# Kernel optimization log

Hardware: AMD Instinct MI355X
Metric: run time of the kernel (lower is better)

## Reference

```python
import jax, jax.numpy as jnp
import numpy as np

B, S, D = 2, 1024, 768
NH = 12
DH = D // NH
HID = 1536
G, EPG = 4, 2
E = G * EPG
TEMP = 1.0
LN_EPS = 1e-5


def setup_inputs() -> dict:
    key = jax.random.key(0)
    ks = jax.random.split(key, 8)
    s = 0.02
    return {
        "x": jax.random.normal(ks[0], (B, S, D), jnp.float32),
        "ln1_w": jnp.ones((D,), jnp.float32),
        "ln1_b": jnp.zeros((D,), jnp.float32),
        "in_proj_w": jax.random.normal(ks[1], (3 * D, D), jnp.float32) * s,
        "in_proj_b": jnp.zeros((3 * D,), jnp.float32),
        "out_proj_w": jax.random.normal(ks[2], (D, D), jnp.float32) * s,
        "out_proj_b": jnp.zeros((D,), jnp.float32),
        "ln2_w": jnp.ones((D,), jnp.float32),
        "ln2_b": jnp.zeros((D,), jnp.float32),
        "Wg": jax.random.normal(ks[3], (D, G), jnp.float32) * s,
        "bg": jnp.zeros((G,), jnp.float32),
        "We": jax.random.normal(ks[4], (G, D, EPG), jnp.float32) * s,
        "be": jnp.zeros((G, EPG), jnp.float32),
        "W1": jax.random.normal(ks[5], (E, D, HID), jnp.float32) * s,
        "b1": jnp.zeros((E, HID), jnp.float32),
        "W2": jax.random.normal(ks[6], (E, HID, D), jnp.float32) * s,
        "b2": jnp.zeros((E, D), jnp.float32),
    }


def _ln(x, w, b):
    m = x.mean(-1, keepdims=True)
    v = x.var(-1, keepdims=True)
    return (x - m) / jnp.sqrt(v + LN_EPS) * w + b


def _mha(h, wqkv, bqkv, wo, bo):
    qkv = h @ wqkv.T + bqkv                       # [B,S,3D]
    q, k, v = jnp.split(qkv, 3, axis=-1)
    q = q.reshape(B, S, NH, DH)
    k = k.reshape(B, S, NH, DH)
    v = v.reshape(B, S, NH, DH)
    scale = 1.0 / np.sqrt(DH).astype(np.float32)
    att = jnp.einsum("bqhd,bkhd->bhqk", q, k) * scale
    p = jax.nn.softmax(att, axis=-1)
    o = jnp.einsum("bhqk,bkhd->bqhd", p, v).reshape(B, S, D)
    return o @ wo.T + bo


def _moe(h, Wg, bg, We, be, W1, b1, W2, b2):
    hf = h.reshape(-1, D)                         # [N,D] tokens
    # level-1: group router (temperature softmax, top-1)
    gp = jax.nn.softmax((hf @ Wg + bg) / TEMP, axis=-1)          # [N,G]
    g = jnp.argmax(gp, axis=-1)                                   # [N]
    pg = jnp.take_along_axis(gp, g[:, None], axis=1)[:, 0]        # [N]
    # level-2: within-group expert router
    el = jnp.einsum("nd,gde->nge", hf, We) + be                   # [N,G,EPG]
    ep = jax.nn.softmax(el / TEMP, axis=-1)
    ep_g = jnp.take_along_axis(ep, g[:, None, None], axis=1)[:, 0, :]  # [N,EPG]
    e = jnp.argmax(ep_g, axis=-1)                                 # [N]
    pe = jnp.take_along_axis(ep_g, e[:, None], axis=1)[:, 0]      # [N]
    flat = g * EPG + e                                            # flat expert id [N]
    combine = jax.nn.one_hot(flat, E, dtype=hf.dtype) * (pg * pe)[:, None]  # [N,E]
    # dense expert compute (reference form of dispatch/grouped-GEMM/combine)
    hid = jax.nn.gelu(jnp.einsum("nd,edh->enh", hf, W1) + b1[:, None, :])   # [E,N,HID]
    y = jnp.einsum("enh,ehd->end", hid, W2) + b2[:, None, :]                # [E,N,D]
    out = jnp.einsum("ne,end->nd", combine, y)                              # [N,D]
    return out.reshape(h.shape)


def reference(x, ln1_w, ln1_b, in_proj_w, in_proj_b, out_proj_w, out_proj_b,
              ln2_w, ln2_b, Wg, bg, We, be, W1, b1, W2, b2):
    a = _mha(_ln(x, ln1_w, ln1_b), in_proj_w, in_proj_b, out_proj_w, out_proj_b)
    x = x + a  # dropout p=0.0 -> identity
    m = _moe(_ln(x, ln2_w, ln2_b), Wg, bg, We, be, W1, b1, W2, b2)
    return x + m
```

## Files before the change

### kernel.cpp

```cpp
#include <hip/hip_runtime.h>
#include <stdint.h>

#define B_ 2
#define S_ 1024
#define D_ 768
#define NH_ 12
#define DH_ 64
#define HID_ 1536
#define G_ 4
#define EPG_ 2
#define E_ 8
#define NTOK (B_*S_)
#define NGRP (B_*NH_*16)

typedef unsigned short u16;
typedef unsigned int u32;
typedef __bf16 bf16x8 __attribute__((ext_vector_type(8)));
typedef float f32x4 __attribute__((ext_vector_type(4)));
typedef u16 u16x4 __attribute__((ext_vector_type(4)));
typedef u32 u32x4 __attribute__((ext_vector_type(4)));

struct BfPair { u16 hi, lo; };

__device__ __forceinline__ u16 f2bf(float f){
// ... 46 lines not shown
    const float* src; u16* dst; int R, C, cx, cy, e;
    if (bid < 11520){
      int r = bid - 2304; e = r / 1152; r %= 1152;
      R = D_; C = HID_; cx = r % 48; cy = r / 48;
      src = W1; dst = W1t;
    } else {
      int r = bid - 11520; e = r / 1152; r %= 1152;
      R = HID_; C = D_; cx = r % 24; cy = r / 24;
      src = W2; dst = W2t;
    }
    const float* s = src + (size_t)e * R * C;
    u16* d = dst + (size_t)e * R * C;
    int c0 = cx * 32, r0 = cy * 32;
    int tx = t & 31, ty = t >> 5;
    #pragma unroll
    for (int i = 0; i < 32; i += 8)
      tile[ty + i][tx] = s[(size_t)(r0 + ty + i) * C + c0 + tx];
    __syncthreads();
    #pragma unroll
    for (int i = 0; i < 32; i += 8)
      d[(size_t)(c0 + ty + i) * R + r0 + tx] = f2bf(tile[tx][ty + i]);
  }
}

__global__ void k_transpose_v(const u16* __restrict__ qh, const u16* __restrict__ ql,
                              u16* __restrict__ vth, u16* __restrict__ vtl){
  __shared__ u16 th[32][34], tl[32][34];
  int bh = blockIdx.z, b = bh / NH_, h = bh % NH_;
  int d0 = blockIdx.x * 32, s0 = blockIdx.y * 32;
  #pragma unroll
  for (int i = 0; i < 32; i += 8){
    size_t src = (size_t)(b * S_ + s0 + threadIdx.y + i) * (3 * D_) + 2 * D_ + h * DH_ + d0 + threadIdx.x;
    th[threadIdx.y + i][threadIdx.x] = qh[src];
    tl[threadIdx.y + i][threadIdx.x] = ql[src];
  }
  __syncthreads();
  #pragma unroll
  for (int i = 0; i < 32; i += 8){
    size_t dst = ((size_t)bh * DH_ + d0 + threadIdx.y + i) * S_ + s0 + threadIdx.x;
    vth[dst] = th[threadIdx.x][threadIdx.y + i];
    vtl[dst] = tl[threadIdx.x][threadIdx.y + i];
  }
}

__global__ __launch_bounds__(256) void k_layernorm(
    const float* __restrict__ x, const float* __restrict__ w, const float* __restrict__ b,
    u16* __restrict__ oh, u16* __restrict__ ol, float* __restrict__ of){
  int row = blockIdx.x;
  const float* xr = x + (size_t)row * D_;
  int t = threadIdx.x;
  float v0 = xr[t], v1 = xr[t + 256], v2 = xr[t + 512];
  float s = v0 + v1 + v2;
  float sq = v0 * v0 + v1 * v1 + v2 * v2;
  #pragma unroll
  for (int m = 1; m < 64; m <<= 1){ s += __shfl_xor(s, m); sq += __shfl_xor(sq, m); }
  __shared__ float ls[4], lq[4];
  int wid = t >> 6;
  if ((t & 63) == 0){ ls[wid] = s; lq[wid] = sq; }
  __syncthreads();
  s = ls[0] + ls[1] + ls[2] + ls[3];
  sq = lq[0] + lq[1] + lq[2] + lq[3];
  float mean = s * (1.f / D_);
  float var = sq * (1.f / D_) - mean * mean;
  float rstd = rsqrtf(var + 1e-5f);
  #pragma unroll
  for (int i = 0; i < 3; i++){
    int dcol = t + i * 256;
    float v = (i == 0 ? v0 : (i == 1 ? v1 : v2));
    float y = (v - mean) * rstd * w[dcol] + b[dcol];
    BfPair p = split_bf(y);
    oh[(size_t)row * D_ + dcol] = p.hi;
    if (ol) ol[(size_t)row * D_ + dcol] = p.lo;
    if (of) of[(size_t)row * D_ + dcol] = y;
  }
}

template<int EPI>
__global__ __launch_bounds__(256) void k_gemm3(
    const u16* __restrict__ Ah, const u16* __restrict__ Al,
    const u16* __restrict__ Bh, const u16* __restrict__ Bl,
    const float* __restrict__ bias, const float* __restrict__ resid,
    u16* __restrict__ outh, u16* __restrict__ outl, float* __restrict__ outf,
    int M, int N, int K){
  __shared__ alignas(16) u16 Ash[2][64 * 32];
  __shared__ alignas(16) u16 Asl[2][64 * 32];
  __shared__ alignas(16) u16 Bsh[2][64 * 32];
  __shared__ alignas(16) u16 Bsl[2][64 * 32];
  int m0 = blockIdx.x * 64, n0 = blockIdx.y * 64;
  int tid = threadIdx.x, w = tid >> 6, l = tid & 63;
  int wr = w >> 1, wc = w & 1;
  f32x4 acc[2][2];
  #pragma unroll
  for (int i = 0; i < 2; i++)
    #pragma unroll
    for (int j = 0; j < 2; j++) acc[i][j] = f32x4{0.f, 0.f, 0.f, 0.f};
  int srow = w * 16 + (l >> 2);
  int scol = 8 * ((l & 3) ^ ((l >> 2) & 3));
  const u16* gAh = Ah + (size_t)(m0 + srow) * K + scol;
  const u16* gAl = Al + (size_t)(m0 + srow) * K + scol;
  const u16* gBh = Bh + (size_t)(n0 + srow) * K + scol;
  const u16* gBl = Bl + (size_t)(n0 + srow) * K + scol;
  int dOff = (w * 16) * 32;
  auto STAGE = [&](int buf, int k0){
    gload_lds16(gAh + k0, &Ash[buf][dOff]);
    gload_lds16(gAl + k0, &Asl[buf][dOff]);
    gload_lds16(gBh + k0, &Bsh[buf][dOff]);
    gload_lds16(gBl + k0, &Bsl[buf][dOff]);
  };
  STAGE(0, 0);
  __syncthreads();
  int nk = K / 32;
  int ca = (l >> 4) ^ (l & 3);
  int ai = (wr * 32 + (l & 15)) * 32 + 8 * ca;
  int bi = (wc * 32 + (l & 15)) * 32 + 8 * ca;
  for (int t = 0; t < nk; t++){
    int cur = t & 1;
    if (t + 1 < nk) STAGE(cur ^ 1, (t + 1) * 32);
    bf16x8 afh[2], afl[2], bfh[2], bfl[2];
    #pragma unroll
    for (int mi = 0; mi < 2; mi++){
      afh[mi] = *(const bf16x8*)&Ash[cur][ai + mi * 16 * 32];
      afl[mi] = *(const bf16x8*)&Asl[cur][ai + mi * 16 * 32];
    }
    #pragma unroll
    for (int ni = 0; ni < 2; ni++){
      bfh[ni] = *(const bf16x8*)&Bsh[cur][bi + ni * 16 * 32];
      bfl[ni] = *(const bf16x8*)&Bsl[cur][bi + ni * 16 * 32];
    }
    #pragma unroll
    for (int mi = 0; mi < 2; mi++)
      #pragma unroll
      for (int ni = 0; ni < 2; ni++){
        acc[mi][ni] = __builtin_amdgcn_mfma_f32_16x16x32_bf16(afh[mi], bfh[ni], acc[mi][ni], 0, 0, 0);
        acc[mi][ni] = __builtin_amdgcn_mfma_f32_16x16x32_bf16(afh[mi], bfl[ni], acc[mi][ni], 0, 0, 0);
        acc[mi][ni] = __builtin_amdgcn_mfma_f32_16x16x32_bf16(afl[mi], bfh[ni], acc[mi][ni], 0, 0, 0);
      }
    __syncthreads();
  }
  int r4 = (l >> 4) * 4, cc = l & 15;
  #pragma unroll
  for (int mi = 0; mi < 2; mi++){
    #pragma unroll
    for (int ni = 0; ni < 2; ni++){
      int col = n0 + wc * 32 + ni * 16 + cc;
      float bv = bias ? bias[col] : 0.f;
      #pragma unroll
      for (int r = 0; r < 4; r++){
        int row = m0 + wr * 32 + mi * 16 + r4 + r;
        float v = acc[mi][ni][r] + bv;
        if (EPI == 0){
          BfPair p = split_bf(v);
          outh[(size_t)row * N + col] = p.hi;
          outl[(size_t)row * N + col] = p.lo;
        } else {
          outf[(size_t)row * N + col] = v + resid[(size_t)row * N + col];
        }
      }
    }
  }
}

__global__ __launch_bounds__(256) void k_attn3(
    const u16* __restrict__ qkvh, const u16* __restrict__ qkvl,
    const u16* __restrict__ vth, const u16* __restrict__ vtl,
    float* __restrict__ po0, float* __restrict__ po1,
    float* __restrict__ pm, float* __restrict__ plsum){
  __shared__ alignas(16) u16 Ksh[2][32 * 64];
  __shared__ alignas(16) u16 Ksl[2][32 * 64];
  __shared__ alignas(16) u16 Vsh[2][64 * 32];
  __shared__ alignas(16) u16 Vsl[2][64 * 32];
  int bh = blockIdx.x, qb = blockIdx.y, ks = blockIdx.z;
  int b = bh / NH_, h = bh % NH_;
  int g = bh * 16 + qb;
  int tid = threadIdx.x, w = tid >> 6, l = tid & 63;
  int q0 = qb * 64 + w * 16;
  const int RS = 3 * D_;
  size_t qoff = (size_t)(b * S_ + q0 + (l & 15)) * RS + h * DH_ + 8 * (l >> 4);
  bf16x8 aqh[2], aql[2];
  aqh[0] = *(const bf16x8*)(qkvh + qoff); aqh[1] = *(const bf16x8*)(qkvh + qoff + 32);
  aql[0] = *(const bf16x8*)(qkvl + qoff); aql[1] = *(const bf16x8*)(qkvl + qoff + 32);
  f32x4 oacc[4];
  #pragma unroll
  for (int i = 0; i < 4; i++) oacc[i] = f32x4{0.f, 0.f, 0.f, 0.f};
  float mrun = -1e30f, lrun = 0.f;

  size_t koff = (size_t)(b * S_ + w * 8 + (l >> 3)) * RS + D_ + h * DH_ + 8 * ((l & 7) ^ (l >> 3));
  const u16* Kgh = qkvh + koff;
  const u16* Kgl = qkvl + koff;
  size_t voff = ((size_t)bh * DH_ + w * 16 + (l >> 2)) * S_ + 8 * ((l & 3) ^ ((l >> 2) & 3));
  const u16* Vgh = vth + voff;
  const u16* Vgl = vtl + voff;
  int wdst = w * 512;

  auto STAGE = [&](int buf, int akt){
    gload_lds16(Kgh + (size_t)(akt * 32) * RS, &Ksh[buf][wdst]);
    gload_lds16(Kgl + (size_t)(akt * 32) * RS, &Ksl[buf][wdst]);
    gload_lds16(Vgh + akt * 32, &Vsh[buf][wdst]);
    gload_lds16(Vgl + akt * 32, &Vsl[buf][wdst]);
  };
  int kt0 = ks * 16;
  STAGE(0, kt0);
  __syncthreads();

  int ck0 = (l >> 4) ^ (l & 7);
  int ck1 = ck0 ^ 4;
  int cv = (l >> 4) ^ (l & 3);
  int s1 = (l & 15) | ((l & 16) << 1);
  int s2 = s1 + 16;
  bool up = (l & 32) != 0;

  for (int kt = 0; kt < 16; kt++){
    int cur = kt & 1;
    if (kt + 1 < 16) STAGE(cur ^ 1, kt0 + kt + 1);
    f32x4 st[2];
    #pragma unroll
    for (int nt = 0; nt < 2; nt++){
      int rbase = (nt * 16 + (l & 15)) * 64;
      bf16x8 kh0 = *(const bf16x8*)&Ksh[cur][rbase + 8 * ck0];
      bf16x8 kh1 = *(const bf16x8*)&Ksh[cur][rbase + 8 * ck1];
      bf16x8 kl0 = *(const bf16x8*)&Ksl[cur][rbase + 8 * ck0];
      bf16x8 kl1 = *(const bf16x8*)&Ksl[cur][rbase + 8 * ck1];
      f32x4 c = f32x4{0.f, 0.f, 0.f, 0.f};
      c = __builtin_amdgcn_mfma_f32_16x16x32_bf16(kh0, aqh[0], c, 0, 0, 0);
      c = __builtin_amdgcn_mfma_f32_16x16x32_bf16(kh1, aqh[1], c, 0, 0, 0);
      c = __builtin_amdgcn_mfma_f32_16x16x32_bf16(kh0, aql[0], c, 0, 0, 0);
      c = __builtin_amdgcn_mfma_f32_16x16x32_bf16(kh1, aql[1], c, 0, 0, 0);
      c = __builtin_amdgcn_mfma_f32_16x16x32_bf16(kl0, aqh[0], c, 0, 0, 0);
      c = __builtin_amdgcn_mfma_f32_16x16x32_bf16(kl1, aqh[1], c, 0, 0, 0);
      st[nt] = c;
    }
    float mx = fmaxf(fmaxf(fmaxf(st[0][0], st[0][1]), fmaxf(st[0][2], st[0][3])),
                     fmaxf(fmaxf(st[1][0], st[1][1]), fmaxf(st[1][2], st[1][3])));
    mx = fmaxf(mx, __shfl_xor(mx, 16));
    mx = fmaxf(mx, __shfl_xor(mx, 32));
    mx *= 0.125f;
    float mnew = fmaxf(mrun, mx);
    float alpha = __expf(mrun - mnew);
    mrun = mnew;
    float p[8]; float sum = 0.f;
    #pragma unroll
    for (int j = 0; j < 8; j++){
      p[j] = __expf(st[j >> 2][j & 3] * 0.125f - mnew);
      sum += p[j];
    }
    sum += __shfl_xor(sum, 16);
    sum += __shfl_xor(sum, 32);
    lrun = lrun * alpha + sum;
    u32 pkh[4], pkl[4];
    #pragma unroll
    for (int i = 0; i < 4; i++){
      BfPair a = split_bf(p[2 * i]), bb = split_bf(p[2 * i + 1]);
      pkh[i] = (u32)a.hi | ((u32)bb.hi << 16);
      pkl[i] = (u32)a.lo | ((u32)bb.lo << 16);
    }
    u32 ah0 = __shfl((int)pkh[0], s1), ah1 = __shfl((int)pkh[1], s1);
    u32 ah2 = __shfl((int)pkh[2], s1), ah3 = __shfl((int)pkh[3], s1);
    u32 bh0 = __shfl((int)pkh[0], s2), bh1 = __shfl((int)pkh[1], s2);
    u32 bh2 = __shfl((int)pkh[2], s2), bh3 = __shfl((int)pkh[3], s2);
    u32 al0 = __shfl((int)pkl[0], s1), al1 = __shfl((int)pkl[1], s1);
    u32 al2 = __shfl((int)pkl[2], s1), al3 = __shfl((int)pkl[3], s1);
    u32 bl0 = __shfl((int)pkl[0], s2), bl1 = __shfl((int)pkl[1], s2);
    u32 bl2 = __shfl((int)pkl[2], s2), bl3 = __shfl((int)pkl[3], s2);
    u32x4 fh, fl;
    fh.x = up ? ah2 : ah0; fh.y = up ? ah3 : ah1; fh.z = up ? bh2 : bh0; fh.w = up ? bh3 : bh1;
    fl.x = up ? al2 : al0; fl.y = up ? al3 : al1; fl.z = up ? bl2 : bl0; fl.w = up ? bl3 : bl1;
    bf16x8 pa_h = __builtin_bit_cast(bf16x8, fh);
    bf16x8 pa_l = __builtin_bit_cast(bf16x8, fl);
    #pragma unroll
    for (int r = 0; r < 4; r++){
      float ar = __shfl(alpha, (l & 48) | (((l >> 4) << 2) + r));
      oacc[0][r] *= ar; oacc[1][r] *= ar; oacc[2][r] *= ar; oacc[3][r] *= ar;
    }
    #pragma unroll
    for (int dt = 0; dt < 4; dt++){
      int vb = (dt * 16 + (l & 15)) * 32 + 8 * cv;
      bf16x8 bvh = *(const bf16x8*)&Vsh[cur][vb];
      bf16x8 bvl = *(const bf16x8*)&Vsl[cur][vb];
      oacc[dt] = __builtin_amdgcn_mfma_f32_16x16x32_bf16(pa_h, bvh, oacc[dt], 0, 0, 0);
      oacc[dt] = __builtin_amdgcn_mfma_f32_16x16x32_bf16(pa_h, bvl, oacc[dt], 0, 0, 0);
      oacc[dt] = __builtin_amdgcn_mfma_f32_16x16x32_bf16(pa_l, bvh, oacc[dt], 0, 0, 0);
    }
    __syncthreads();
  }
  float* po = ks ? po1 : po0;
  #pragma unroll
  for (int dt = 0; dt < 4; dt++)
    #pragma unroll
    for (int r = 0; r < 4; r++){
      int qloc = w * 16 + (l >> 4) * 4 + r;
      int d = dt * 16 + (l & 15);
      po[((size_t)(g * 64 + qloc)) * 64 + d] = oacc[dt][r];
    }
  if (l < 16){
    pm[(ks * NGRP + g) * 64 + w * 16 + l] = mrun;
    plsum[(ks * NGRP + g) * 64 + w * 16 + l] = lrun;
  }
}

__global__ __launch_bounds__(256) void k_attn_merge(
    const float* __restrict__ po0, const float* __restrict__ po1,
    const float* __restrict__ pm, const float* __restrict__ plsum,
    u16* __restrict__ oh, u16* __restrict__ ol){
  int bh = blockIdx.x, qb = blockIdx.y;
  int b = bh / NH_, h = bh % NH_;
  int g = bh * 16 + qb;
  int t = threadIdx.x;
  int q = t >> 2, d0 = (t & 3) * 16;
  float m0 = pm[g * 64 + q],      m1 = pm[NGRP * 64 + g * 64 + q];
  float l0 = plsum[g * 64 + q],   l1 = plsum[NGRP * 64 + g * 64 + q];
  float M = fmaxf(m0, m1);
  float a0 = __expf(m0 - M), a1 = __expf(m1 - M);
  float rcp = 1.f / (l0 * a0 + l1 * a1);
  size_t base = ((size_t)(g * 64 + q)) * 64 + d0;
  size_t orow = (size_t)(b * S_ + qb * 64 + q) * D_ + h * DH_ + d0;
  #pragma unroll
  for (int j = 0; j < 16; j++){
    float v = (po0[base + j] * a0 + po1[base + j] * a1) * rcp;
    BfPair p = split_bf(v);
    oh[orow + j] = p.hi;
    ol[orow + j] = p.lo;
  }
}

__global__ __launch_bounds__(256) void k_router(
    const float* __restrict__ h2f, const float* __restrict__ Wg, const float* __restrict__ bg,
    const float* __restrict__ We, const float* __restrict__ be,
    int* __restrict__ flat, float* __restrict__ pc){
  int w = threadIdx.x >> 6, l = threadIdx.x & 63;
  int n = blockIdx.x * 4 + w;
  const float* hr = h2f + (size_t)n * D_;
  float pl[4] = {0.f, 0.f, 0.f, 0.f};
  for (int d = l; d < D_; d += 64){
    float hv = hr[d];
    float4 wg = *(const float4*)&Wg[d * 4];
    pl[0] += hv * wg.x; pl[1] += hv * wg.y; pl[2] += hv * wg.z; pl[3] += hv * wg.w;
  }
  #pragma unroll
  for (int m = 1; m < 64; m <<= 1)
    #pragma unroll
    for (int g = 0; g < 4; g++) pl[g] += __shfl_xor(pl[g], m);
  float lg[4];
  #pragma unroll
  for (int g = 0; g < 4; g++) lg[g] = pl[g] + bg[g];
  int gi = 0; float gm = lg[0];
  #pragma unroll
  for (int g = 1; g < 4; g++) if (lg[g] > gm){ gm = lg[g]; gi = g; }
  float gs = 0.f;
  #pragma unroll
  for (int g = 0; g < 4; g++) gs += expf(lg[g] - gm);
  float pg = 1.f / gs;
  float e0 = 0.f, e1 = 0.f;
  for (int d = l; d < D_; d += 64){
    float hv = hr[d];
    float2 we = *(const float2*)&We[((size_t)gi * D_ + d) * 2];
    e0 += hv * we.x; e1 += hv * we.y;
  }
  #pragma unroll
  for (int m = 1; m < 64; m <<= 1){ e0 += __shfl_xor(e0, m); e1 += __shfl_xor(e1, m); }
  e0 += be[gi * 2]; e1 += be[gi * 2 + 1];
  int ei; float pe;
  if (e1 > e0){ ei = 1; pe = 1.f / (1.f + expf(e0 - e1)); }
  else        { ei = 0; pe = 1.f / (1.f + expf(e1 - e0)); }
  if (l == 0){
    flat[n] = gi * 2 + ei;
    pc[n] = pg * pe;
// ... 165 lines not shown
        acc[mi][ni] = __builtin_amdgcn_mfma_f32_16x16x32_bf16(af[mi][1], bfr[ni][1], acc[mi][ni], 0, 0, 0);
      }
    __syncthreads();
  }
  int r4 = (l >> 4) * 4, cc = l & 15;
  #pragma unroll
  for (int mi = 0; mi < 2; mi++){
    #pragma unroll
    for (int r = 0; r < 4; r++){
      int rowl = mt * 64 + wr * 32 + mi * 16 + r4 + r;
      if (rowl < cnt){
        int tok = order[off + rowl];
        float pv = pc[tok];
        #pragma unroll
        for (int ni = 0; ni < 2; ni++){
          int col = nt * 64 + wc * 32 + ni * 16 + cc;
          float v = acc[mi][ni][r] + b2[e * D_ + col];
          out[(size_t)tok * D_ + col] = x2[(size_t)tok * D_ + col] + pv * v;
        }
      }
    }
  }
}

extern "C" void kernel_launch(void* const* d_in, const int* in_sizes, int n_in,
                              void* d_out, int out_size, void* d_ws, size_t ws_size,
                              hipStream_t stream){
  const float* x         = (const float*)d_in[0];
  const float* ln1_w     = (const float*)d_in[1];
  const float* ln1_b     = (const float*)d_in[2];
  const float* in_proj_w = (const float*)d_in[3];
  const float* in_proj_b = (const float*)d_in[4];
  const float* out_proj_w= (const float*)d_in[5];
  const float* out_proj_b= (const float*)d_in[6];
  const float* ln2_w     = (const float*)d_in[7];
  const float* ln2_b     = (const float*)d_in[8];
  const float* Wg        = (const float*)d_in[9];
  const float* bg        = (const float*)d_in[10];
  const float* We        = (const float*)d_in[11];
  const float* be        = (const float*)d_in[12];
  const float* W1        = (const float*)d_in[13];
  const float* b1        = (const float*)d_in[14];
  const float* W2        = (const float*)d_in[15];
  const float* b2        = (const float*)d_in[16];
  float* out = (float*)d_out;

  char* ws = (char*)d_ws;
  size_t off = 0;
  auto alloc = [&](size_t bytes) -> char* {
    char* p = ws + off;
    off += (bytes + 255) & ~(size_t)255;
    return p;
  };
  u16*   inpTh = (u16*)  alloc((size_t)3 * D_ * D_ * 2);
  u16*   inpTl = (u16*)  alloc((size_t)3 * D_ * D_ * 2);
  u16*   outpTh= (u16*)  alloc((size_t)D_ * D_ * 2);
  u16*   outpTl= (u16*)  alloc((size_t)D_ * D_ * 2);
  u16*   W1t  = (u16*)  alloc((size_t)E_ * HID_ * D_ * 2);
  u16*   W2t  = (u16*)  alloc((size_t)E_ * D_ * HID_ * 2);
  u16*   qkvh = (u16*)  alloc((size_t)NTOK * 3 * D_ * 2);
  u16*   qkvl = (u16*)  alloc((size_t)NTOK * 3 * D_ * 2);
  u16*   h1h  = (u16*)  alloc((size_t)NTOK * D_ * 2);
  u16*   h1l  = (u16*)  alloc((size_t)NTOK * D_ * 2);
  u16*   vth  = (u16*)  alloc((size_t)B_ * NH_ * DH_ * S_ * 2);
  u16*   vtl  = (u16*)  alloc((size_t)B_ * NH_ * DH_ * S_ * 2);
  float* x2   = (float*)alloc((size_t)NTOK * D_ * 4);
  u16*   h2   = (u16*)  alloc((size_t)NTOK * D_ * 2);
  int*   flat = (int*)  alloc(NTOK * 4);
  float* pc   = (float*)alloc(NTOK * 4);
  int*   order= (int*)  alloc(NTOK * 4);
  int*   moeI = (int*)  alloc(32 * 4);
  float* po0  = (float*)h1h;
  float* po1  = (float*)inpTh;
  float* pmArr= (float*)((char*)inpTh + 6291456);
  float* plArr= (float*)((char*)inpTh + 6291456 + 196608);
  u16*   attnh= qkvh;
  u16*   attnl= qkvl;
  float* h2f  = (float*)qkvh;
  u16*   hid  = (u16*)qkvl;

  k_prep<<<dim3(20736), dim3(256), 0, stream>>>(
      in_proj_w, out_proj_w, W1, W2, inpTh, inpTl, outpTh, outpTl, W1t, W2t);
  k_layernorm<<<dim3(NTOK), dim3(256), 0, stream>>>(x, ln1_w, ln1_b, h1h, h1l, (float*)nullptr);
  k_gemm3<0><<<dim3(NTOK / 64, 3 * D_ / 64), dim3(256), 0, stream>>>(
      h1h, h1l, inpTh, inpTl, in_proj_b, nullptr, qkvh, qkvl, nullptr, NTOK, 3 * D_, D_);
  k_transpose_v<<<dim3(DH_ / 32, S_ / 32, B_ * NH_), dim3(32, 8), 0, stream>>>(qkvh, qkvl, vth, vtl);
  k_attn3<<<dim3(B_ * NH_, S_ / 64, 2), dim3(256), 0, stream>>>(
      qkvh, qkvl, vth, vtl, po0, po1, pmArr, plArr);
  k_attn_merge<<<dim3(B_ * NH_, S_ / 64), dim3(256), 0, stream>>>(
      po0, po1, pmArr, plArr, attnh, attnl);
  k_gemm3<1><<<dim3(NTOK / 64, D_ / 64), dim3(256), 0, stream>>>(
      attnh, attnl, outpTh, outpTl, out_proj_b, x, nullptr, nullptr, x2, NTOK, D_, D_);
  k_layernorm<<<dim3(NTOK), dim3(256), 0, stream>>>(x2, ln2_w, ln2_b, h2, (u16*)nullptr, h2f);
  k_router<<<dim3(NTOK / 4), dim3(256), 0, stream>>>(h2f, Wg, bg, We, be, flat, pc);
  k_bucket<<<dim3(1), dim3(1024), 0, stream>>>(flat, moeI, order);
  k_moe_gemm1<<<dim3(E_, NTOK / 64, HID_ / 64), dim3(256), 0, stream>>>(h2, W1t, b1, order, moeI, hid);
  k_moe_gemm2<<<dim3(E_, NTOK / 64, D_ / 64), dim3(256), 0, stream>>>(hid, W2t, b2, order, moeI, pc, x2, out);
}
```

Baseline: 207.1 us.

## Enlarge GEMM M-tile to 128 and load attention K/V fragments directly from global

The split-bf16 GEMM now computes a 128x64 tile per block, each wave owning 32 rows by 64 columns, which halves the grid and reuses B fragments across more rows. The attention kernel drops its LDS staging and barriers, loading K and V MFMA fragments straight from global memory into registers with one-tile-ahead K prefetch. It also skips the online-softmax rescale when no row max increases. This trades fewer syncs and better reuse for more register pressure, fewer blocks per GEMM, and uncoalesced or duplicated global reads in attention.

```diff
diff --git a/kernel.cpp b/kernel.cpp
--- a/kernel.cpp
+++ b/kernel.cpp
@@ -152,55 +152,58 @@
     const float* __restrict__ bias, const float* __restrict__ resid,
     u16* __restrict__ outh, u16* __restrict__ outl, float* __restrict__ outf,
     int M, int N, int K){
-  __shared__ alignas(16) u16 Ash[2][64 * 32];
-  __shared__ alignas(16) u16 Asl[2][64 * 32];
+  __shared__ alignas(16) u16 Ash[2][128 * 32];
+  __shared__ alignas(16) u16 Asl[2][128 * 32];
   __shared__ alignas(16) u16 Bsh[2][64 * 32];
   __shared__ alignas(16) u16 Bsl[2][64 * 32];
-  int m0 = blockIdx.x * 64, n0 = blockIdx.y * 64;
+  int m0 = blockIdx.x * 128, n0 = blockIdx.y * 64;
   int tid = threadIdx.x, w = tid >> 6, l = tid & 63;
-  int wr = w >> 1, wc = w & 1;
-  f32x4 acc[2][2];
+  f32x4 acc[2][4];
   #pragma unroll
   for (int i = 0; i < 2; i++)
     #pragma unroll
-    for (int j = 0; j < 2; j++) acc[i][j] = f32x4{0.f, 0.f, 0.f, 0.f};
-  int srow = w * 16 + (l >> 2);
+    for (int j = 0; j < 4; j++) acc[i][j] = f32x4{0.f, 0.f, 0.f, 0.f};
+  int srow = l >> 2;
   int scol = 8 * ((l & 3) ^ ((l >> 2) & 3));
-  const u16* gAh = Ah + (size_t)(m0 + srow) * K + scol;
-  const u16* gAl = Al + (size_t)(m0 + srow) * K + scol;
-  const u16* gBh = Bh + (size_t)(n0 + srow) * K + scol;
-  const u16* gBl = Bl + (size_t)(n0 + srow) * K + scol;
-  int dOff = (w * 16) * 32;
+  const u16* gAh0 = Ah + (size_t)(m0 + w * 32 + srow) * K + scol;
+  const u16* gAh1 = gAh0 + (size_t)16 * K;
+  const u16* gAl0 = Al + (size_t)(m0 + w * 32 + srow) * K + scol;
+  const u16* gAl1 = gAl0 + (size_t)16 * K;
+  const u16* gBh = Bh + (size_t)(n0 + w * 16 + srow) * K + scol;
+  const u16* gBl = Bl + (size_t)(n0 + w * 16 + srow) * K + scol;
+  int dA0 = (w * 32) * 32, dA1 = (w * 32 + 16) * 32, dB = (w * 16) * 32;
   auto STAGE = [&](int buf, int k0){
-    gload_lds16(gAh + k0, &Ash[buf][dOff]);
-    gload_lds16(gAl + k0, &Asl[buf][dOff]);
-    gload_lds16(gBh + k0, &Bsh[buf][dOff]);
-    gload_lds16(gBl + k0, &Bsl[buf][dOff]);
+    gload_lds16(gAh0 + k0, &Ash[buf][dA0]);
+    gload_lds16(gAh1 + k0, &Ash[buf][dA1]);
+    gload_lds16(gAl0 + k0, &Asl[buf][dA0]);
+    gload_lds16(gAl1 + k0, &Asl[buf][dA1]);
+    gload_lds16(gBh + k0, &Bsh[buf][dB]);
+    gload_lds16(gBl + k0, &Bsl[buf][dB]);
   };
   STAGE(0, 0);
   __syncthreads();
   int nk = K / 32;
   int ca = (l >> 4) ^ (l & 3);
-  int ai = (wr * 32 + (l & 15)) * 32 + 8 * ca;
-  int bi = (wc * 32 + (l & 15)) * 32 + 8 * ca;
+  int ai0 = (w * 32 + (l & 15)) * 32 + 8 * ca;
+  int ai1 = ai0 + 16 * 32;
   for (int t = 0; t < nk; t++){
     int cur = t & 1;
     if (t + 1 < nk) STAGE(cur ^ 1, (t + 1) * 32);
-    bf16x8 afh[2], afl[2], bfh[2], bfl[2];
-    #pragma unroll
-    for (int mi = 0; mi < 2; mi++){
-      afh[mi] = *(const bf16x8*)&Ash[cur][ai + mi * 16 * 32];
-      afl[mi] = *(const bf16x8*)&Asl[cur][ai + mi * 16 * 32];
-    }
-    #pragma unroll
-    for (int ni = 0; ni < 2; ni++){
-      bfh[ni] = *(const bf16x8*)&Bsh[cur][bi + ni * 16 * 32];
-      bfl[ni] = *(const bf16x8*)&Bsl[cur][bi + ni * 16 * 32];
+    bf16x8 afh[2], afl[2], bfh[4], bfl[4];
+    afh[0] = *(const bf16x8*)&Ash[cur][ai0];
+    afh[1] = *(const bf16x8*)&Ash[cur][ai1];
+    afl[0] = *(const bf16x8*)&Asl[cur][ai0];
+    afl[1] = *(const bf16x8*)&Asl[cur][ai1];
+    #pragma unroll
+    for (int ni = 0; ni < 4; ni++){
+      int bi = (ni * 16 + (l & 15)) * 32 + 8 * ca;
+      bfh[ni] = *(const bf16x8*)&Bsh[cur][bi];
+      bfl[ni] = *(const bf16x8*)&Bsl[cur][bi];
     }
     #pragma unroll
     for (int mi = 0; mi < 2; mi++)
       #pragma unroll
-      for (int ni = 0; ni < 2; ni++){
+      for (int ni = 0; ni < 4; ni++){
         acc[mi][ni] = __builtin_amdgcn_mfma_f32_16x16x32_bf16(afh[mi], bfh[ni], acc[mi][ni], 0, 0, 0);
         acc[mi][ni] = __builtin_amdgcn_mfma_f32_16x16x32_bf16(afh[mi], bfl[ni], acc[mi][ni], 0, 0, 0);
         acc[mi][ni] = __builtin_amdgcn_mfma_f32_16x16x32_bf16(afl[mi], bfh[ni], acc[mi][ni], 0, 0, 0);
@@ -211,12 +214,12 @@
   #pragma unroll
   for (int mi = 0; mi < 2; mi++){
     #pragma unroll
-    for (int ni = 0; ni < 2; ni++){
-      int col = n0 + wc * 32 + ni * 16 + cc;
+    for (int ni = 0; ni < 4; ni++){
+      int col = n0 + ni * 16 + cc;
       float bv = bias ? bias[col] : 0.f;
       #pragma unroll
       for (int r = 0; r < 4; r++){
-        int row = m0 + wr * 32 + mi * 16 + r4 + r;
+        int row = m0 + w * 32 + mi * 16 + r4 + r;
         float v = acc[mi][ni][r] + bv;
         if (EPI == 0){
           BfPair p = split_bf(v);
@@ -230,15 +233,14 @@
   }
 }
 
+struct KF { bf16x8 h00, h01, h10, h11, l00, l01, l10, l11; };
+struct VF { bf16x8 h0, h1, h2, h3, l0, l1, l2, l3; };
+
 __global__ __launch_bounds__(256) void k_attn3(
     const u16* __restrict__ qkvh, const u16* __restrict__ qkvl,
     const u16* __restrict__ vth, const u16* __restrict__ vtl,
     float* __restrict__ po0, float* __restrict__ po1,
     float* __restrict__ pm, float* __restrict__ plsum){
-  __shared__ alignas(16) u16 Ksh[2][32 * 64];
-  __shared__ alignas(16) u16 Ksl[2][32 * 64];
-  __shared__ alignas(16) u16 Vsh[2][64 * 32];
-  __shared__ alignas(16) u16 Vsl[2][64 * 32];
   int bh = blockIdx.x, qb = blockIdx.y, ks = blockIdx.z;
   int b = bh / NH_, h = bh % NH_;
   int g = bh * 16 + qb;
@@ -246,76 +248,89 @@
   int q0 = qb * 64 + w * 16;
   const int RS = 3 * D_;
   size_t qoff = (size_t)(b * S_ + q0 + (l & 15)) * RS + h * DH_ + 8 * (l >> 4);
-  bf16x8 aqh[2], aql[2];
-  aqh[0] = *(const bf16x8*)(qkvh + qoff); aqh[1] = *(const bf16x8*)(qkvh + qoff + 32);
-  aql[0] = *(const bf16x8*)(qkvl + qoff); aql[1] = *(const bf16x8*)(qkvl + qoff + 32);
+  bf16x8 aqh0 = *(const bf16x8*)(qkvh + qoff), aqh1 = *(const bf16x8*)(qkvh + qoff + 32);
+  bf16x8 aql0 = *(const bf16x8*)(qkvl + qoff), aql1 = *(const bf16x8*)(qkvl + qoff + 32);
   f32x4 oacc[4];
   #pragma unroll
   for (int i = 0; i < 4; i++) oacc[i] = f32x4{0.f, 0.f, 0.f, 0.f};
   float mrun = -1e30f, lrun = 0.f;
 
-  size_t koff = (size_t)(b * S_ + w * 8 + (l >> 3)) * RS + D_ + h * DH_ + 8 * ((l & 7) ^ (l >> 3));
-  const u16* Kgh = qkvh + koff;
-  const u16* Kgl = qkvl + koff;
-  size_t voff = ((size_t)bh * DH_ + w * 16 + (l >> 2)) * S_ + 8 * ((l & 3) ^ ((l >> 2) & 3));
-  const u16* Vgh = vth + voff;
-  const u16* Vgl = vtl + voff;
-  int wdst = w * 512;
-
-  auto STAGE = [&](int buf, int akt){
-    gload_lds16(Kgh + (size_t)(akt * 32) * RS, &Ksh[buf][wdst]);
-    gload_lds16(Kgl + (size_t)(akt * 32) * RS, &Ksl[buf][wdst]);
-    gload_lds16(Vgh + akt * 32, &Vsh[buf][wdst]);
-    gload_lds16(Vgl + akt * 32, &Vsl[buf][wdst]);
+  const u16* Kbh = qkvh + (size_t)(b * S_ + (l & 15)) * RS + D_ + h * DH_ + 8 * (l >> 4);
+  const u16* Kbl = qkvl + (size_t)(b * S_ + (l & 15)) * RS + D_ + h * DH_ + 8 * (l >> 4);
+  const u16* Vbh = vth + ((size_t)bh * DH_ + (l & 15)) * S_ + 8 * (l >> 4);
+  const u16* Vbl = vtl + ((size_t)bh * DH_ + (l & 15)) * S_ + 8 * (l >> 4);
+
+  auto loadK = [&](int kt) -> KF {
+    KF k;
+    size_t o0 = (size_t)(kt * 32) * RS, o1 = (size_t)(kt * 32 + 16) * RS;
+    k.h00 = *(const bf16x8*)(Kbh + o0);      k.h01 = *(const bf16x8*)(Kbh + o0 + 32);
+    k.h10 = *(const bf16x8*)(Kbh + o1);      k.h11 = *(const bf16x8*)(Kbh + o1 + 32);
+    k.l00 = *(const bf16x8*)(Kbl + o0);      k.l01 = *(const bf16x8*)(Kbl + o0 + 32);
+    k.l10 = *(const bf16x8*)(Kbl + o1);      k.l11 = *(const bf16x8*)(Kbl + o1 + 32);
+    return k;
   };
-  int kt0 = ks * 16;
-  STAGE(0, kt0);
-  __syncthreads();
-
-  int ck0 = (l >> 4) ^ (l & 7);
-  int ck1 = ck0 ^ 4;
-  int cv = (l >> 4) ^ (l & 3);
+  auto loadV = [&](int kt) -> VF {
+    VF v;
+    int o = kt * 32;
+    v.h0 = *(const bf16x8*)(Vbh + o);
+    v.h1 = *(const bf16x8*)(Vbh + o + 16 * S_);
+    v.h2 = *(const bf16x8*)(Vbh + o + 32 * S_);
+    v.h3 = *(const bf16x8*)(Vbh + o + 48 * S_);
+    v.l0 = *(const bf16x8*)(Vbl + o);
+    v.l1 = *(const bf16x8*)(Vbl + o + 16 * S_);
+    v.l2 = *(const bf16x8*)(Vbl + o + 32 * S_);
+    v.l3 = *(const bf16x8*)(Vbl + o + 48 * S_);
+    return v;
+  };
+
   int s1 = (l & 15) | ((l & 16) << 1);
   int s2 = s1 + 16;
   bool up = (l & 32) != 0;
 
-  for (int kt = 0; kt < 16; kt++){
-    int cur = kt & 1;
-    if (kt + 1 < 16) STAGE(cur ^ 1, kt0 + kt + 1);
-    f32x4 st[2];
-    #pragma unroll
-    for (int nt = 0; nt < 2; nt++){
-      int rbase = (nt * 16 + (l & 15)) * 64;
-      bf16x8 kh0 = *(const bf16x8*)&Ksh[cur][rbase + 8 * ck0];
-      bf16x8 kh1 = *(const bf16x8*)&Ksh[cur][rbase + 8 * ck1];
-      bf16x8 kl0 = *(const bf16x8*)&Ksl[cur][rbase + 8 * ck0];
-      bf16x8 kl1 = *(const bf16x8*)&Ksl[cur][rbase + 8 * ck1];
-      f32x4 c = f32x4{0.f, 0.f, 0.f, 0.f};
-      c = __builtin_amdgcn_mfma_f32_16x16x32_bf16(kh0, aqh[0], c, 0, 0, 0);
-      c = __builtin_amdgcn_mfma_f32_16x16x32_bf16(kh1, aqh[1], c, 0, 0, 0);
-      c = __builtin_amdgcn_mfma_f32_16x16x32_bf16(kh0, aql[0], c, 0, 0, 0);
-      c = __builtin_amdgcn_mfma_f32_16x16x32_bf16(kh1, aql[1], c, 0, 0, 0);
-      c = __builtin_amdgcn_mfma_f32_16x16x32_bf16(kl0, aqh[0], c, 0, 0, 0);
-      c = __builtin_amdgcn_mfma_f32_16x16x32_bf16(kl1, aqh[1], c, 0, 0, 0);
-      st[nt] = c;
-    }
-    float mx = fmaxf(fmaxf(fmaxf(st[0][0], st[0][1]), fmaxf(st[0][2], st[0][3])),
-                     fmaxf(fmaxf(st[1][0], st[1][1]), fmaxf(st[1][2], st[1][3])));
+  int kt0 = ks * 16, ktE = kt0 + 16;
+  KF kc = loadK(kt0);
+  for (int kt = kt0; kt < ktE; kt++){
+    VF vf = loadV(kt);
+    KF kn = loadK(kt + 1 < ktE ? kt + 1 : kt);
+    f32x4 st0 = f32x4{0.f, 0.f, 0.f, 0.f}, st1 = f32x4{0.f, 0.f, 0.f, 0.f};
+    st0 = __builtin_amdgcn_mfma_f32_16x16x32_bf16(kc.h00, aqh0, st0, 0, 0, 0);
+    st0 = __builtin_amdgcn_mfma_f32_16x16x32_bf16(kc.h01, aqh1, st0, 0, 0, 0);
+    st0 = __builtin_amdgcn_mfma_f32_16x16x32_bf16(kc.h00, aql0, st0, 0, 0, 0);
+    st0 = __builtin_amdgcn_mfma_f32_16x16x32_bf16(kc.h01, aql1, st0, 0, 0, 0);
+    st0 = __builtin_amdgcn_mfma_f32_16x16x32_bf16(kc.l00, aqh0, st0, 0, 0, 0);
+    st0 = __builtin_amdgcn_mfma_f32_16x16x32_bf16(kc.l01, aqh1, st0, 0, 0, 0);
+    st1 = __builtin_amdgcn_mfma_f32_16x16x32_bf16(kc.h10, aqh0, st1, 0, 0, 0);
+    st1 = __builtin_amdgcn_mfma_f32_16x16x32_bf16(kc.h11, aqh1, st1, 0, 0, 0);
+    st1 = __builtin_amdgcn_mfma_f32_16x16x32_bf16(kc.h10, aql0, st1, 0, 0, 0);
+    st1 = __builtin_amdgcn_mfma_f32_16x16x32_bf16(kc.h11, aql1, st1, 0, 0, 0);
+    st1 = __builtin_amdgcn_mfma_f32_16x16x32_bf16(kc.l10, aqh0, st1, 0, 0, 0);
+    st1 = __builtin_amdgcn_mfma_f32_16x16x32_bf16(kc.l11, aqh1, st1, 0, 0, 0);
+    float mx = fmaxf(fmaxf(fmaxf(st0[0], st0[1]), fmaxf(st0[2], st0[3])),
+                     fmaxf(fmaxf(st1[0], st1[1]), fmaxf(st1[2], st1[3])));
     mx = fmaxf(mx, __shfl_xor(mx, 16));
     mx = fmaxf(mx, __shfl_xor(mx, 32));
     mx *= 0.125f;
-    float mnew = fmaxf(mrun, mx);
-    float alpha = __expf(mrun - mnew);
-    mrun = mnew;
+    if (!__all(mx <= mrun)){
+      float mnew = fmaxf(mrun, mx);
+      float alpha = __expf(mrun - mnew);
+      lrun *= alpha;
+      #pragma unroll
+      for (int r = 0; r < 4; r++){
+        float ar = __shfl(alpha, (l & 48) | (((l >> 4) << 2) + r));
+        oacc[0][r] *= ar; oacc[1][r] *= ar; oacc[2][r] *= ar; oacc[3][r] *= ar;
+      }
+      mrun = mnew;
+    }
     float p[8]; float sum = 0.f;
     #pragma unroll
     for (int j = 0; j < 8; j++){
-      p[j] = __expf(st[j >> 2][j & 3] * 0.125f - mnew);
+      float sv = (j < 4) ? st0[j & 3] : st1[j & 3];
+      p[j] = __expf(sv * 0.125f - mrun);
       sum += p[j];
     }
     sum += __shfl_xor(sum, 16);
     sum += __shfl_xor(sum, 32);
-    lrun = lrun * alpha + sum;
+    lrun += sum;
     u32 pkh[4], pkl[4];
     #pragma unroll
     for (int i = 0; i < 4; i++){
@@ -336,21 +351,19 @@
     fl.x = up ? al2 : al0; fl.y = up ? al3 : al1; fl.z = up ? bl2 : bl0; fl.w = up ? bl3 : bl1;
     bf16x8 pa_h = __builtin_bit_cast(bf16x8, fh);
     bf16x8 pa_l = __builtin_bit_cast(bf16x8, fl);
-    #pragma unroll
-    for (int r = 0; r < 4; r++){
-      float ar = __shfl(alpha, (l & 48) | (((l >> 4) << 2) + r));
-      oacc[0][r] *= ar; oacc[1][r] *= ar; oacc[2][r] *= ar; oacc[3][r] *= ar;
-    }
-    #pragma unroll
-    for (int dt = 0; dt < 4; dt++){
-      int vb = (dt * 16 + (l & 15)) * 32 + 8 * cv;
-      bf16x8 bvh = *(const bf16x8*)&Vsh[cur][vb];
-      bf16x8 bvl = *(const bf16x8*)&Vsl[cur][vb];
-      oacc[dt] = __builtin_amdgcn_mfma_f32_16x16x32_bf16(pa_h, bvh, oacc[dt], 0, 0, 0);
-      oacc[dt] = __builtin_amdgcn_mfma_f32_16x16x32_bf16(pa_h, bvl, oacc[dt], 0, 0, 0);
-      oacc[dt] = __builtin_amdgcn_mfma_f32_16x16x32_bf16(pa_l, bvh, oacc[dt], 0, 0, 0);
-    }
-    __syncthreads();
+    oacc[0] = __builtin_amdgcn_mfma_f32_16x16x32_bf16(pa_h, vf.h0, oacc[0], 0, 0, 0);
+    oacc[0] = __builtin_amdgcn_mfma_f32_16x16x32_bf16(pa_h, vf.l0, oacc[0], 0, 0, 0);
+    oacc[0] = __builtin_amdgcn_mfma_f32_16x16x32_bf16(pa_l, vf.h0, oacc[0], 0, 0, 0);
+    oacc[1] = __builtin_amdgcn_mfma_f32_16x16x32_bf16(pa_h, vf.h1, oacc[1], 0, 0, 0);
+    oacc[1] = __builtin_amdgcn_mfma_f32_16x16x32_bf16(pa_h, vf.l1, oacc[1], 0, 0, 0);
+    oacc[1] = __builtin_amdgcn_mfma_f32_16x16x32_bf16(pa_l, vf.h1, oacc[1], 0, 0, 0);
+    oacc[2] = __builtin_amdgcn_mfma_f32_16x16x32_bf16(pa_h, vf.h2, oacc[2], 0, 0, 0);
+    oacc[2] = __builtin_amdgcn_mfma_f32_16x16x32_bf16(pa_h, vf.l2, oacc[2], 0, 0, 0);
+    oacc[2] = __builtin_amdgcn_mfma_f32_16x16x32_bf16(pa_l, vf.h2, oacc[2], 0, 0, 0);
+    oacc[3] = __builtin_amdgcn_mfma_f32_16x16x32_bf16(pa_h, vf.h3, oacc[3], 0, 0, 0);
+    oacc[3] = __builtin_amdgcn_mfma_f32_16x16x32_bf16(pa_h, vf.l3, oacc[3], 0, 0, 0);
+    oacc[3] = __builtin_amdgcn_mfma_f32_16x16x32_bf16(pa_l, vf.h3, oacc[3], 0, 0, 0);
+    kc = kn;
   }
   float* po = ks ? po1 : po0;
   #pragma unroll
@@ -682,14 +695,14 @@
   k_prep<<<dim3(20736), dim3(256), 0, stream>>>(
       in_proj_w, out_proj_w, W1, W2, inpTh, inpTl, outpTh, outpTl, W1t, W2t);
   k_layernorm<<<dim3(NTOK), dim3(256), 0, stream>>>(x, ln1_w, ln1_b, h1h, h1l, (float*)nullptr);
-  k_gemm3<0><<<dim3(NTOK / 64, 3 * D_ / 64), dim3(256), 0, stream>>>(
+  k_gemm3<0><<<dim3(NTOK / 128, 3 * D_ / 64), dim3(256), 0, stream>>>(
       h1h, h1l, inpTh, inpTl, in_proj_b, nullptr, qkvh, qkvl, nullptr, NTOK, 3 * D_, D_);
   k_transpose_v<<<dim3(DH_ / 32, S_ / 32, B_ * NH_), dim3(32, 8), 0, stream>>>(qkvh, qkvl, vth, vtl);
   k_attn3<<<dim3(B_ * NH_, S_ / 64, 2), dim3(256), 0, stream>>>(
       qkvh, qkvl, vth, vtl, po0, po1, pmArr, plArr);
   k_attn_merge<<<dim3(B_ * NH_, S_ / 64), dim3(256), 0, stream>>>(
       po0, po1, pmArr, plArr, attnh, attnl);
-  k_gemm3<1><<<dim3(NTOK / 64, D_ / 64), dim3(256), 0, stream>>>(
+  k_gemm3<1><<<dim3(NTOK / 128, D_ / 64), dim3(256), 0, stream>>>(
       attnh, attnl, outpTh, outpTl, out_proj_b, x, nullptr, nullptr, x2, NTOK, D_, D_);
   k_layernorm<<<dim3(NTOK), dim3(256), 0, stream>>>(x2, ln2_w, ln2_b, h2, (u16*)nullptr, h2f);
   k_router<<<dim3(NTOK / 4), dim3(256), 0, stream>>>(h2f, Wg, bg, We, be, flat, pc);
```

Result: slower. 260.1 us (+25.6%).

## Enlarge split-bf16 GEMM tile to 128x64 and skip redundant softmax rescales

Applied to the files above, without the earlier changes.

The QKV and out-projection GEMM now uses a 128x64 block tile, with each wave computing a 32x64 sub-tile instead of 32x32. This raises B-fragment reuse per wave and halves the block count, at the cost of more LDS, registers and fewer blocks for small grids. Separately, the flash-attention loop now rescales the running output and sum only when some lane's row max actually grows. That skips the exp, shuffles and multiplies on most iterations but adds a wave-wide vote and a branch.

```diff
diff --git a/kernel.cpp b/kernel.cpp
--- a/kernel.cpp
+++ b/kernel.cpp
@@ -152,55 +152,58 @@
     const float* __restrict__ bias, const float* __restrict__ resid,
     u16* __restrict__ outh, u16* __restrict__ outl, float* __restrict__ outf,
     int M, int N, int K){
-  __shared__ alignas(16) u16 Ash[2][64 * 32];
-  __shared__ alignas(16) u16 Asl[2][64 * 32];
+  __shared__ alignas(16) u16 Ash[2][128 * 32];
+  __shared__ alignas(16) u16 Asl[2][128 * 32];
   __shared__ alignas(16) u16 Bsh[2][64 * 32];
   __shared__ alignas(16) u16 Bsl[2][64 * 32];
-  int m0 = blockIdx.x * 64, n0 = blockIdx.y * 64;
+  int m0 = blockIdx.x * 128, n0 = blockIdx.y * 64;
   int tid = threadIdx.x, w = tid >> 6, l = tid & 63;
-  int wr = w >> 1, wc = w & 1;
-  f32x4 acc[2][2];
+  f32x4 acc[2][4];
   #pragma unroll
   for (int i = 0; i < 2; i++)
     #pragma unroll
-    for (int j = 0; j < 2; j++) acc[i][j] = f32x4{0.f, 0.f, 0.f, 0.f};
-  int srow = w * 16 + (l >> 2);
+    for (int j = 0; j < 4; j++) acc[i][j] = f32x4{0.f, 0.f, 0.f, 0.f};
+  int srow = l >> 2;
   int scol = 8 * ((l & 3) ^ ((l >> 2) & 3));
-  const u16* gAh = Ah + (size_t)(m0 + srow) * K + scol;
-  const u16* gAl = Al + (size_t)(m0 + srow) * K + scol;
-  const u16* gBh = Bh + (size_t)(n0 + srow) * K + scol;
-  const u16* gBl = Bl + (size_t)(n0 + srow) * K + scol;
-  int dOff = (w * 16) * 32;
+  const u16* gAh0 = Ah + (size_t)(m0 + w * 32 + srow) * K + scol;
+  const u16* gAh1 = gAh0 + (size_t)16 * K;
+  const u16* gAl0 = Al + (size_t)(m0 + w * 32 + srow) * K + scol;
+  const u16* gAl1 = gAl0 + (size_t)16 * K;
+  const u16* gBh = Bh + (size_t)(n0 + w * 16 + srow) * K + scol;
+  const u16* gBl = Bl + (size_t)(n0 + w * 16 + srow) * K + scol;
+  int dA0 = (w * 32) * 32, dA1 = (w * 32 + 16) * 32, dB = (w * 16) * 32;
   auto STAGE = [&](int buf, int k0){
-    gload_lds16(gAh + k0, &Ash[buf][dOff]);
-    gload_lds16(gAl + k0, &Asl[buf][dOff]);
-    gload_lds16(gBh + k0, &Bsh[buf][dOff]);
-    gload_lds16(gBl + k0, &Bsl[buf][dOff]);
+    gload_lds16(gAh0 + k0, &Ash[buf][dA0]);
+    gload_lds16(gAh1 + k0, &Ash[buf][dA1]);
+    gload_lds16(gAl0 + k0, &Asl[buf][dA0]);
+    gload_lds16(gAl1 + k0, &Asl[buf][dA1]);
+    gload_lds16(gBh + k0, &Bsh[buf][dB]);
+    gload_lds16(gBl + k0, &Bsl[buf][dB]);
   };
   STAGE(0, 0);
   __syncthreads();
   int nk = K / 32;
   int ca = (l >> 4) ^ (l & 3);
-  int ai = (wr * 32 + (l & 15)) * 32 + 8 * ca;
-  int bi = (wc * 32 + (l & 15)) * 32 + 8 * ca;
+  int ai0 = (w * 32 + (l & 15)) * 32 + 8 * ca;
+  int ai1 = ai0 + 16 * 32;
   for (int t = 0; t < nk; t++){
     int cur = t & 1;
     if (t + 1 < nk) STAGE(cur ^ 1, (t + 1) * 32);
-    bf16x8 afh[2], afl[2], bfh[2], bfl[2];
-    #pragma unroll
-    for (int mi = 0; mi < 2; mi++){
-      afh[mi] = *(const bf16x8*)&Ash[cur][ai + mi * 16 * 32];
-      afl[mi] = *(const bf16x8*)&Asl[cur][ai + mi * 16 * 32];
-    }
-    #pragma unroll
-    for (int ni = 0; ni < 2; ni++){
-      bfh[ni] = *(const bf16x8*)&Bsh[cur][bi + ni * 16 * 32];
-      bfl[ni] = *(const bf16x8*)&Bsl[cur][bi + ni * 16 * 32];
+    bf16x8 afh[2], afl[2], bfh[4], bfl[4];
+    afh[0] = *(const bf16x8*)&Ash[cur][ai0];
+    afh[1] = *(const bf16x8*)&Ash[cur][ai1];
+    afl[0] = *(const bf16x8*)&Asl[cur][ai0];
+    afl[1] = *(const bf16x8*)&Asl[cur][ai1];
+    #pragma unroll
+    for (int ni = 0; ni < 4; ni++){
+      int bi = (ni * 16 + (l & 15)) * 32 + 8 * ca;
+      bfh[ni] = *(const bf16x8*)&Bsh[cur][bi];
+      bfl[ni] = *(const bf16x8*)&Bsl[cur][bi];
     }
     #pragma unroll
     for (int mi = 0; mi < 2; mi++)
       #pragma unroll
-      for (int ni = 0; ni < 2; ni++){
+      for (int ni = 0; ni < 4; ni++){
         acc[mi][ni] = __builtin_amdgcn_mfma_f32_16x16x32_bf16(afh[mi], bfh[ni], acc[mi][ni], 0, 0, 0);
         acc[mi][ni] = __builtin_amdgcn_mfma_f32_16x16x32_bf16(afh[mi], bfl[ni], acc[mi][ni], 0, 0, 0);
         acc[mi][ni] = __builtin_amdgcn_mfma_f32_16x16x32_bf16(afl[mi], bfh[ni], acc[mi][ni], 0, 0, 0);
@@ -211,12 +214,12 @@
   #pragma unroll
   for (int mi = 0; mi < 2; mi++){
     #pragma unroll
-    for (int ni = 0; ni < 2; ni++){
-      int col = n0 + wc * 32 + ni * 16 + cc;
+    for (int ni = 0; ni < 4; ni++){
+      int col = n0 + ni * 16 + cc;
       float bv = bias ? bias[col] : 0.f;
       #pragma unroll
       for (int r = 0; r < 4; r++){
-        int row = m0 + wr * 32 + mi * 16 + r4 + r;
+        int row = m0 + w * 32 + mi * 16 + r4 + r;
         float v = acc[mi][ni][r] + bv;
         if (EPI == 0){
           BfPair p = split_bf(v);
@@ -304,18 +307,26 @@
     mx = fmaxf(mx, __shfl_xor(mx, 16));
     mx = fmaxf(mx, __shfl_xor(mx, 32));
     mx *= 0.125f;
-    float mnew = fmaxf(mrun, mx);
-    float alpha = __expf(mrun - mnew);
-    mrun = mnew;
+    if (!__all(mx <= mrun)){
+      float mnew = fmaxf(mrun, mx);
+      float alpha = __expf(mrun - mnew);
+      lrun *= alpha;
+      #pragma unroll
+      for (int r = 0; r < 4; r++){
+        float ar = __shfl(alpha, (l & 48) | (((l >> 4) << 2) + r));
+        oacc[0][r] *= ar; oacc[1][r] *= ar; oacc[2][r] *= ar; oacc[3][r] *= ar;
+      }
+      mrun = mnew;
+    }
     float p[8]; float sum = 0.f;
     #pragma unroll
     for (int j = 0; j < 8; j++){
-      p[j] = __expf(st[j >> 2][j & 3] * 0.125f - mnew);
+      p[j] = __expf(st[j >> 2][j & 3] * 0.125f - mrun);
       sum += p[j];
     }
     sum += __shfl_xor(sum, 16);
     sum += __shfl_xor(sum, 32);
-    lrun = lrun * alpha + sum;
+    lrun += sum;
     u32 pkh[4], pkl[4];
     #pragma unroll
     for (int i = 0; i < 4; i++){
@@ -336,11 +347,6 @@
     fl.x = up ? al2 : al0; fl.y = up ? al3 : al1; fl.z = up ? bl2 : bl0; fl.w = up ? bl3 : bl1;
     bf16x8 pa_h = __builtin_bit_cast(bf16x8, fh);
     bf16x8 pa_l = __builtin_bit_cast(bf16x8, fl);
-    #pragma unroll
-    for (int r = 0; r < 4; r++){
-      float ar = __shfl(alpha, (l & 48) | (((l >> 4) << 2) + r));
-      oacc[0][r] *= ar; oacc[1][r] *= ar; oacc[2][r] *= ar; oacc[3][r] *= ar;
-    }
     #pragma unroll
     for (int dt = 0; dt < 4; dt++){
       int vb = (dt * 16 + (l & 15)) * 32 + 8 * cv;
@@ -682,14 +688,14 @@
   k_prep<<<dim3(20736), dim3(256), 0, stream>>>(
       in_proj_w, out_proj_w, W1, W2, inpTh, inpTl, outpTh, outpTl, W1t, W2t);
   k_layernorm<<<dim3(NTOK), dim3(256), 0, stream>>>(x, ln1_w, ln1_b, h1h, h1l, (float*)nullptr);
-  k_gemm3<0><<<dim3(NTOK / 64, 3 * D_ / 64), dim3(256), 0, stream>>>(
+  k_gemm3<0><<<dim3(NTOK / 128, 3 * D_ / 64), dim3(256), 0, stream>>>(
       h1h, h1l, inpTh, inpTl, in_proj_b, nullptr, qkvh, qkvl, nullptr, NTOK, 3 * D_, D_);
   k_transpose_v<<<dim3(DH_ / 32, S_ / 32, B_ * NH_), dim3(32, 8), 0, stream>>>(qkvh, qkvl, vth, vtl);
   k_attn3<<<dim3(B_ * NH_, S_ / 64, 2), dim3(256), 0, stream>>>(
       qkvh, qkvl, vth, vtl, po0, po1, pmArr, plArr);
   k_attn_merge<<<dim3(B_ * NH_, S_ / 64), dim3(256), 0, stream>>>(
       po0, po1, pmArr, plArr, attnh, attnl);
-  k_gemm3<1><<<dim3(NTOK / 64, D_ / 64), dim3(256), 0, stream>>>(
+  k_gemm3<1><<<dim3(NTOK / 128, D_ / 64), dim3(256), 0, stream>>>(
       attnh, attnl, outpTh, outpTl, out_proj_b, x, nullptr, nullptr, x2, NTOK, D_, D_);
   k_layernorm<<<dim3(NTOK), dim3(256), 0, stream>>>(x2, ln2_w, ln2_b, h2, (u16*)nullptr, h2f);
   k_router<<<dim3(NTOK / 4), dim3(256), 0, stream>>>(h2f, Wg, bg, We, be, flat, pc);
```

Result: no change. 209.7 us (+1.3%).
